# Kernel optimization log

Measured on AMD Instinct MI355X. Metric: run time of the kernel, lower is better.

Reference implementation:

```python
import jax, jax.numpy as jnp
import numpy as np

D_MODEL = 512
N_HEADS = 8
HEAD_DIM = D_MODEL // N_HEADS
D_FF = 2048
EPS = 1e-5


def layer_norm(x, gamma, beta):
    mu = jnp.mean(x, axis=-1, keepdims=True)
    var = jnp.mean((x - mu) ** 2, axis=-1, keepdims=True)
    return (x - mu) * jax.lax.rsqrt(var + EPS) * gamma + beta


def setup_inputs() -> dict:
    key = jax.random.key(0)
    ks = jax.random.split(key, 17)
    B, S = 2, 2048
    s_in = 1.0 / np.sqrt(D_MODEL)
    s_ff = 1.0 / np.sqrt(D_FF)
    return {
        "x": jax.random.normal(ks[0], (B, S, D_MODEL), jnp.float32),
        "Wq": jax.random.normal(ks[1], (D_MODEL, D_MODEL), jnp.float32) * s_in,
        "bq": jnp.zeros((D_MODEL,), jnp.float32),
        "Wk": jax.random.normal(ks[2], (D_MODEL, D_MODEL), jnp.float32) * s_in,
        "bk": jnp.zeros((D_MODEL,), jnp.float32),
        "Wv": jax.random.normal(ks[3], (D_MODEL, D_MODEL), jnp.float32) * s_in,
        "bv": jnp.zeros((D_MODEL,), jnp.float32),
        "Wo": jax.random.normal(ks[4], (D_MODEL, D_MODEL), jnp.float32) * s_in,
        "bo": jnp.zeros((D_MODEL,), jnp.float32),
        "W1": jax.random.normal(ks[5], (D_MODEL, D_FF), jnp.float32) * s_in,
        "b1": jnp.zeros((D_FF,), jnp.float32),
        "W2": jax.random.normal(ks[6], (D_FF, D_MODEL), jnp.float32) * s_ff,
        "b2": jnp.zeros((D_MODEL,), jnp.float32),
        "g1": jnp.ones((D_MODEL,), jnp.float32),
        "be1": jnp.zeros((D_MODEL,), jnp.float32),
        "g2": jnp.ones((D_MODEL,), jnp.float32),
        "be2": jnp.zeros((D_MODEL,), jnp.float32),
    }


def reference(x, Wq, bq, Wk, bk, Wv, bv, Wo, bo, W1, b1, W2, b2, g1, be1, g2, be2):
    B, S, _ = x.shape
    # projections + split heads -> [B, H, S, Dh]
    def heads(t):
        return t.reshape(B, S, N_HEADS, HEAD_DIM).transpose(0, 2, 1, 3)
    q = heads(x @ Wq + bq)
    k = heads(x @ Wk + bk)
    v = heads(x @ Wv + bv)
    # explicit scaled dot-product attention (full [B,H,S,S] scores as in source)
    scores = jnp.einsum('bhqd,bhkd->bhqk', q, k) / np.sqrt(HEAD_DIM).astype(np.float32)
    attn = jax.nn.softmax(scores, axis=-1)
    ctx = jnp.einsum('bhqk,bhkd->bhqd', attn, v)
    ctx = ctx.transpose(0, 2, 1, 3).reshape(B, S, D_MODEL)
    attn_out = ctx @ Wo + bo
    # post-norm residual 1
    h = layer_norm(x + attn_out, g1, be1)
    # FFN
    ff = jax.nn.relu(h @ W1 + b1) @ W2 + b2
    # post-norm residual 2
    return layer_norm(h + ff, g2, be2)
```

## Files before the change

### kernel.cpp

```cpp
#include <hip/hip_runtime.h>
#include <cmath>

#define D_MODEL 512
#define N_HEADS 8
#define HEAD_DIM 64
#define D_FF 2048
#define SEQ 2048
#define BATCH 2
#define MROWS (BATCH * SEQ)

typedef __attribute__((ext_vector_type(8))) short short8;
typedef __attribute__((ext_vector_type(4))) float float4v;
typedef unsigned short ushort_t;

static __device__ __forceinline__ ushort_t f2bf(float f) {
    union { float f; unsigned u; } v; v.f = f;
    unsigned r = (v.u + 0x7FFFu + ((v.u >> 16) & 1u)) >> 16;
    return (ushort_t)r;
}
static __device__ __forceinline__ ushort_t f2bf_trunc(float f) {
    union { float f; unsigned u; } v; v.f = f;
    return (ushort_t)(v.u >> 16);
}

static __device__ __forceinline__ void gload16(const void* g, void* l) {
    __builtin_amdgcn_global_load_lds(
        (__attribute__((address_space(1))) void*)(unsigned long long)g,
        (__attribute__((address_space(3))) void*)(unsigned)(unsigned long long)l,
        16, 0, 0);
}

__global__ __launch_bounds__(256) void xbf_k(const float* __restrict__ x,
                                             ushort_t* __restrict__ xb)
{
    int i = blockIdx.x * 256 + threadIdx.x;
    float4 f = ((const float4*)x)[i];
    ushort4 o;
    o.x = f2bf(f.x); o.y = f2bf(f.y); o.z = f2bf(f.z); o.w = f2bf(f.w);
    ((ushort4*)xb)[i] = o;
}

__global__ __launch_bounds__(256) void wt_k(
    const float* __restrict__ Wq, const float* __restrict__ Wk,
    const float* __restrict__ Wv, const float* __restrict__ Wo,
    const float* __restrict__ W1, const float* __restrict__ W2,
    ushort_t* __restrict__ WqkvT, ushort_t* __restrict__ WoT,
    ushort_t* __restrict__ W1T, ushort_t* __restrict__ W2T)
{
    int tile = blockIdx.x;
    const float* src; ushort_t* dst; int Kd, Nd, tloc;
    if (tile < 1024) {
        int wsel = tile >> 8; tloc = tile & 255; Kd = 512; Nd = 512;
        if (wsel == 0)      { src = Wq; dst = WqkvT; }
        else if (wsel == 1) { src = Wk; dst = WqkvT + (size_t)512 * 512; }
        else if (wsel == 2) { src = Wv; dst = WqkvT + (size_t)1024 * 512; }
        else                { src = Wo; dst = WoT; }
    } else if (tile < 2048) { tloc = tile - 1024; Kd = 512;  Nd = 2048; src = W1; dst = W1T; }
    else                    { tloc = tile - 2048; Kd = 2048; Nd = 512;  src = W2; dst = W2T; }
    int tn = Nd >> 5;
    int k0 = (tloc / tn) << 5, n0 = (tloc % tn) << 5;
    __shared__ float tl[32][33];
    int c = threadIdx.x & 31, r = threadIdx.x >> 5;
    #pragma unroll
    for (int i = 0; i < 4; ++i)
        tl[r + i * 8][c] = src[(size_t)(k0 + r + i * 8) * Nd + n0 + c];
    __syncthreads();
    #pragma unroll
    for (int i = 0; i < 4; ++i)
        dst[(size_t)(n0 + r + i * 8) * Kd + k0 + c] = f2bf(tl[c][r + i * 8]);
}

template <int BM, int BN, int WCOLS, int MT, int NT>
__device__ __forceinline__ void gemm_core(
    const ushort_t* __restrict__ A, const ushort_t* __restrict__ BT,
    int K, int kbase, int Klen, int m0, int n0, float4v (&acc)[MT][NT])
{
    __shared__ ushort_t As[BM * 32];
    __shared__ ushort_t Bs[BN * 32];

    const int t = threadIdx.x;
    const int w = t >> 6;
    const int lane = t & 63;
    const int l16 = lane & 15;
    const int quad = lane >> 4;
    const int mbase = (w / WCOLS) * (MT * 16);
    const int nbase = (w % WCOLS) * (NT * 16);
    const int lr = lane >> 2;
    const int lc = (lane & 3) * 8;

    for (int k0 = kbase; k0 < kbase + Klen; k0 += 32) {
        __syncthreads();
        for (int c = w; c < BM / 16; c += 4)
            gload16(A + (size_t)(m0 + c * 16 + lr) * K + k0 + lc, &As[c * 512]);
        for (int c = w; c < BN / 16; c += 4)
            gload16(BT + (size_t)(n0 + c * 16 + lr) * K + k0 + lc, &Bs[c * 512]);
        __syncthreads();

        short8 af[MT], bfr[NT];
        #pragma unroll
        for (int mt = 0; mt < MT; ++mt)
            af[mt] = *(const short8*)&As[(mbase + mt * 16 + l16) * 32 + quad * 8];
        #pragma unroll
        for (int nt = 0; nt < NT; ++nt)
            bfr[nt] = *(const short8*)&Bs[(nbase + nt * 16 + l16) * 32 + quad * 8];
        #pragma unroll
        for (int mt = 0; mt < MT; ++mt)
            #pragma unroll
            for (int nt = 0; nt < NT; ++nt)
                acc[mt][nt] = __builtin_amdgcn_mfma_f32_16x16x32_bf16(
                    af[mt], bfr[nt], acc[mt][nt], 0, 0, 0);
    }
}

template <int BM, int BN, int WCOLS, int MT, int NT, int MODE>
__global__ __launch_bounds__(256) void gemm_std_k(
    const ushort_t* __restrict__ A, const ushort_t* __restrict__ BT,
    const float* __restrict__ bias, void* __restrict__ Cv,
    int N, int K, int Klen, size_t zstride)
{
    const int m0 = blockIdx.y * BM;
    const int n0 = blockIdx.x * BN;
    const int kbase = blockIdx.z * Klen;
    float4v acc[MT][NT];
    #pragma unroll
    for (int mt = 0; mt < MT; ++mt)
        #pragma unroll
        for (int nt = 0; nt < NT; ++nt)
            acc[mt][nt] = (float4v){0.f, 0.f, 0.f, 0.f};
    gemm_core<BM, BN, WCOLS, MT, NT>(A, BT, K, kbase, Klen, m0, n0, acc);

    const int t = threadIdx.x;
    const int w = t >> 6, lane = t & 63, l16 = lane & 15, quad = lane >> 4;
    const int mbase = (w / WCOLS) * (MT * 16);
    const int nbase = (w % WCOLS) * (NT * 16);
    float* Cf = (float*)Cv + blockIdx.z * zstride;
    #pragma unroll
    for (int mt = 0; mt < MT; ++mt) {
        #pragma unroll
        for (int nt = 0; nt < NT; ++nt) {
            int gcol = n0 + nbase + nt * 16 + l16;
            float b = (MODE == 2) ? 0.f : bias[gcol];
            #pragma unroll
            for (int r = 0; r < 4; ++r) {
                int grow = m0 + mbase + mt * 16 + quad * 4 + r;
                float v = acc[mt][nt][r] + b;
                if (MODE == 1) v = fmaxf(v, 0.f);
                if (MODE == 1) ((ushort_t*)Cv)[(size_t)grow * N + gcol] = f2bf(v);
                else           Cf[(size_t)grow * N + gcol] = v;
            }
        }
    }
}

__global__ __launch_bounds__(256) void gemm_qkv_k(
    const ushort_t* __restrict__ A, const ushort_t* __restrict__ BT,
    const float* __restrict__ bq, const float* __restrict__ bk,
    const float* __restrict__ bv,
    ushort_t* __restrict__ Qb, ushort_t* __restrict__ Kb,
    ushort_t* __restrict__ VTb)
{
    const int m0 = blockIdx.y * 64;
    const int n0 = blockIdx.x * 128;
    float4v acc[2][4];
    #pragma unroll
    for (int mt = 0; mt < 2; ++mt)
        #pragma unroll
        for (int nt = 0; nt < 4; ++nt)
            acc[mt][nt] = (float4v){0.f, 0.f, 0.f, 0.f};
    gemm_core<64, 128, 2, 2, 4>(A, BT, 512, 0, 512, m0, n0, acc);

    const int t = threadIdx.x;
    const int w = t >> 6, lane = t & 63, l16 = lane & 15, quad = lane >> 4;
    const int mbase = (w >> 1) * 32;
    const int nbase = (w & 1) * 64;
    const int tsel = n0 >> 9;
    const float* bias = (tsel == 0) ? bq : (tsel == 1) ? bk : bv;
    const float scl = (tsel == 0) ? 0.18033688f : 1.0f;
    ushort_t* dst = (tsel == 0) ? Qb : Kb;

    #pragma unroll
    for (int mt = 0; mt < 2; ++mt) {
        #pragma unroll
        for (int nt = 0; nt < 4; ++nt) {
            int gcol = n0 + nbase + nt * 16 + l16;
            int lcol = gcol - (tsel << 9);
            int h = lcol >> 6, dh = lcol & 63;
            float b = bias[lcol];
            #pragma unroll
            for (int r = 0; r < 4; ++r) {
                int grow = m0 + mbase + mt * 16 + quad * 4 + r;
                int bb = grow >> 11, s = grow & 2047;
                float v = (acc[mt][nt][r] + b) * scl;
                if (tsel < 2)
                    dst[(((size_t)(bb * N_HEADS + h)) * SEQ + s) * HEAD_DIM + dh] = f2bf(v);
                else
                    VTb[(((size_t)(bb * N_HEADS + h)) * HEAD_DIM + dh) * SEQ + s] = f2bf(v);
            }
        }
    }
}

__global__ __launch_bounds__(256) void attn_mfma_k(
    const ushort_t* __restrict__ Qg, const ushort_t* __restrict__ Kg,
    const ushort_t* __restrict__ VTg,
    float* __restrict__ Opart, float* __restrict__ Lpart)
{
    __shared__ __align__(16) ushort_t Ks[64 * 72];
    __shared__ __align__(16) ushort_t Vs[64 * 72];
    __shared__ __align__(16) ushort_t Ps[4][16 * 76];

    const int bh = blockIdx.x;
    const int q0 = blockIdx.y * 64;
    const int ks = blockIdx.z;
    const int t = threadIdx.x;
    const int w = t >> 6;
    const int lane = t & 63;
    const int l16 = lane & 15;
    const int quad = lane >> 4;
    const int qbase = q0 + w * 16;
    const float M2 = 14.4269504f;

    short8 aq[2];
    {
        const ushort_t* qp = Qg + ((size_t)bh * SEQ + qbase + l16) * HEAD_DIM + quad * 8;
        aq[0] = *(const short8*)(qp);
        aq[1] = *(const short8*)(qp + 32);
    }

    float4v o[4] = {};
    float l_acc[4] = {0.f, 0.f, 0.f, 0.f};

    for (int kt = 0; kt < 16; ++kt) {
        const int kbase = ks * 1024 + kt * 64;
        __syncthreads();
        #pragma unroll
        for (int lit = 0; lit < 2; ++lit) {
            int flat = lit * 256 + t;
            int row = flat >> 3;
            int c0 = (flat & 7) * 8;
            *(short8*)&Ks[row * 72 + c0] =
                *(const short8*)(Kg + ((size_t)bh * SEQ + kbase + row) * HEAD_DIM + c0);
            *(short8*)&Vs[row * 72 + c0] =
                *(const short8*)(VTg + ((size_t)bh * HEAD_DIM + row) * SEQ + kbase + c0);
        }
        __syncthreads();

        float4v s[4];
        #pragma unroll
        for (int nt = 0; nt < 4; ++nt) s[nt] = (float4v){0.f, 0.f, 0.f, 0.f};
        #pragma unroll
        for (int c = 0; c < 2; ++c) {
            #pragma unroll
            for (int nt = 0; nt < 4; ++nt) {
                short8 bk8 = *(const short8*)&Ks[(nt * 16 + l16) * 72 + c * 32 + quad * 8];
                s[nt] = __builtin_amdgcn_mfma_f32_16x16x32_bf16(aq[c], bk8, s[nt], 0, 0, 0);
            }
        }

        #pragma unroll
        for (int nt = 0; nt < 4; ++nt) {
            #pragma unroll
            for (int r = 0; r < 4; ++r) {
                float p = exp2f(s[nt][r] - M2);
                s[nt][r] = p;
                l_acc[r] += p;
            }
        }

        #pragma unroll
        for (int nt = 0; nt < 4; ++nt)
            #pragma unroll
            for (int r = 0; r < 4; ++r)
                Ps[w][(quad * 4 + r) * 76 + nt * 16 + l16] = f2bf_trunc(s[nt][r]);
        asm volatile("s_waitcnt lgkmcnt(0)" ::: "memory");

        #pragma unroll
        for (int c = 0; c < 2; ++c) {
            short8 ap = *(const short8*)&Ps[w][l16 * 76 + c * 32 + quad * 8];
            #pragma unroll
            for (int dt = 0; dt < 4; ++dt) {
                short8 bv8 = *(const short8*)&Vs[(dt * 16 + l16) * 72 + c * 32 + quad * 8];
                o[dt] = __builtin_amdgcn_mfma_f32_16x16x32_bf16(ap, bv8, o[dt], 0, 0, 0);
            }
        }
    }

    const size_t pbase = ((size_t)(ks * 16 + bh)) * SEQ;
    #pragma unroll
    for (int r = 0; r < 4; ++r) {
        float L = l_acc[r];
        #pragma unroll
        for (int msk = 1; msk < 16; msk <<= 1) L += __shfl_xor(L, msk);
        int qrow = qbase + quad * 4 + r;
        if (l16 == 0) Lpart[pbase + qrow] = L;
        #pragma unroll
        for (int dt = 0; dt < 4; ++dt)
            Opart[(pbase + qrow) * HEAD_DIM + dt * 16 + l16] = o[dt][r];
    }
}

__global__ __launch_bounds__(256) void attn_comb_k(
    const float* __restrict__ Op, const float* __restrict__ Lp,
    ushort_t* __restrict__ ctx)
{
    int g = blockIdx.x * 256 + threadIdx.x;
    int d4 = g & 15;
    int q  = (g >> 4) & 2047;
    int bh = g >> 15;
    size_t rowa = ((size_t)bh * SEQ + q) * HEAD_DIM;
    size_t rowb = ((size_t)(16 + bh) * SEQ + q) * HEAD_DIM;
    float4 a = ((const float4*)(Op + rowa))[d4];
    float4 b = ((const float4*)(Op + rowb))[d4];
    float inv = 1.0f / (Lp[bh * SEQ + q] + Lp[16 * SEQ + bh * SEQ + q]);
    ushort4 o4;
    o4.x = f2bf((a.x + b.x) * inv);
    o4.y = f2bf((a.y + b.y) * inv);
    o4.z = f2bf((a.z + b.z) * inv);
    o4.w = f2bf((a.w + b.w) * inv);
    int bb = bh >> 3, hh = bh & 7;
    *(ushort4*)&ctx[((size_t)(bb * SEQ + q)) * D_MODEL + hh * HEAD_DIM + d4 * 4] = o4;
}

template <int WRITE_BF>
__global__ __launch_bounds__(256) void add_ln_k(
    const float* __restrict__ X, const float* __restrict__ P0,
    const float* __restrict__ P1, const float* __restrict__ bias,
    const float* __restrict__ gam, const float* __restrict__ bet,
    float* __restrict__ O, ushort_t* __restrict__ Ob)
{
    const int row = blockIdx.x;
    const int t = threadIdx.x;
    const size_t ro = (size_t)row * D_MODEL;

    float v0 = X[ro + t]       + P0[ro + t]       + P1[ro + t]       + bias[t];
    float v1 = X[ro + t + 256] + P0[ro + t + 256] + P1[ro + t + 256] + bias[t + 256];
    float s = v0 + v1;
    float ss = v0 * v0 + v1 * v1;
    #pragma unroll
    for (int off = 32; off > 0; off >>= 1) {
        s  += __shfl_down(s, off);
        ss += __shfl_down(ss, off);
    }
    __shared__ float sb[4], ssb[4];
    if ((t & 63) == 0) { sb[t >> 6] = s; ssb[t >> 6] = ss; }
    __syncthreads();
    float S  = sb[0] + sb[1] + sb[2] + sb[3];
    float SS = ssb[0] + ssb[1] + ssb[2] + ssb[3];
    float mu  = S * (1.0f / D_MODEL);
    float var = SS * (1.0f / D_MODEL) - mu * mu;
    float inv = rsqrtf(var + 1e-5f);
    float o0 = (v0 - mu) * inv * gam[t] + bet[t];
    float o1 = (v1 - mu) * inv * gam[t + 256] + bet[t + 256];
    O[ro + t]       = o0;
    O[ro + t + 256] = o1;
    if (WRITE_BF) {
        Ob[ro + t]       = f2bf(o0);
        Ob[ro + t + 256] = f2bf(o1);
    }
}

extern "C" void kernel_launch(void* const* d_in, const int* in_sizes, int n_in,
                              void* d_out, int out_size, void* d_ws, size_t ws_size,
                              hipStream_t stream)
{
    const float* x   = (const float*)d_in[0];
    const float* Wq  = (const float*)d_in[1];
    const float* bq  = (const float*)d_in[2];
    const float* Wk  = (const float*)d_in[3];
    const float* bk  = (const float*)d_in[4];
    const float* Wv  = (const float*)d_in[5];
    const float* bv  = (const float*)d_in[6];
    const float* Wo  = (const float*)d_in[7];
    const float* bo  = (const float*)d_in[8];
    const float* W1  = (const float*)d_in[9];
    const float* b1  = (const float*)d_in[10];
    const float* W2  = (const float*)d_in[11];
    const float* b2  = (const float*)d_in[12];
    const float* g1  = (const float*)d_in[13];
    const float* be1 = (const float*)d_in[14];
    const float* g2  = (const float*)d_in[15];
    const float* be2 = (const float*)d_in[16];
    float* out = (float*)d_out;
    float* ws  = (float*)d_ws;

    ushort_t* WoT   = (ushort_t*)(ws);
    ushort_t* W1T   = (ushort_t*)(ws + 131072);
    ushort_t* W2T   = (ushort_t*)(ws + 655360);
    ushort_t* WqkvT = (ushort_t*)(ws + 1179648);
    ushort_t* xb    = (ushort_t*)(ws + 1572864);
    ushort_t* Qb    = (ushort_t*)(ws + 2621440);
    ushort_t* Kb    = (ushort_t*)(ws + 3670016);
    ushort_t* VTb   = (ushort_t*)(ws + 4718592);
    ushort_t* Ctx   = (ushort_t*)(ws + 5767168);
    float*    Lpart = ws + 6815744;
    float*    Hh    = ws + 6881280;
    float*    P0    = ws + 8978432;
    float*    P1    = ws + 11075584;
    float*    Opart = ws + 8978432;
    ushort_t* FF1   = (ushort_t*)(ws + 1572864);
    ushort_t* Hhb   = (ushort_t*)(ws + 5767168);

    xbf_k<<<2048, 256, 0, stream>>>(x, xb);
    wt_k<<<3072, 256, 0, stream>>>(Wq, Wk, Wv, Wo, W1, W2, WqkvT, WoT, W1T, W2T);

    gemm_qkv_k<<<dim3(12, 64), 256, 0, stream>>>(xb, WqkvT, bq, bk, bv, Qb, Kb, VTb);

    attn_mfma_k<<<dim3(16, 32, 2), 256, 0, stream>>>(Qb, Kb, VTb, Opart, Lpart);
    attn_comb_k<<<2048, 256, 0, stream>>>(Opart, Lpart, Ctx);

    gemm_std_k<64, 64, 2, 2, 2, 2><<<dim3(8, 64, 2), 256, 0, stream>>>(
        Ctx, WoT, nullptr, P0, 512, 512, 256, (size_t)MROWS * D_MODEL);

    add_ln_k<1><<<4096, 256, 0, stream>>>(x, P0, P1, bo, g1, be1, Hh, Hhb);

    gemm_std_k<64, 128, 2, 2, 4, 1><<<dim3(16, 64), 256, 0, stream>>>(
        Hhb, W1T, b1, FF1, 2048, 512, 512, 0);

    gemm_std_k<64, 64, 2, 2, 2, 2><<<dim3(8, 64, 2), 256, 0, stream>>>(
        FF1, W2T, nullptr, P0, 512, 2048, 1024, (size_t)MROWS * D_MODEL);

    add_ln_k<0><<<4096, 256, 0, stream>>>(Hh, P0, P1, b2, g2, be2, out, (ushort_t*)nullptr);
}
```

Before: 232.7 us.

## Replace LDS GEMMs with direct-load register-pipelined GEMMs, split attention keys four ways

Several changes land together. The weight-transpose and x-to-bf16 kernels are merged into a single prep launch. Every GEMM drops the LDS-staged core in favour of wave-private direct global loads into registers, double-buffered across k steps (32x256 block tiles). The key split in attention goes from 2 to 4 partitions, with a matching 4-way combine, and the P scratch in LDS uses an XOR swizzle in place of padding. The workspace offsets are moved so the larger Opart buffer fits. The aim is to cut launch count, barrier overhead and LDS bank conflicts and to raise attention parallelism. The cost is that A and B operands are no longer shared through LDS, so the GEMMs issue more redundant global and L2 reads, and the combine pass moves more partial data.

```diff
diff --git a/kernel.cpp b/kernel.cpp
--- a/kernel.cpp
+++ b/kernel.cpp
@@ -23,31 +23,24 @@
     return (ushort_t)(v.u >> 16);
 }
 
-static __device__ __forceinline__ void gload16(const void* g, void* l) {
-    __builtin_amdgcn_global_load_lds(
-        (__attribute__((address_space(1))) void*)(unsigned long long)g,
-        (__attribute__((address_space(3))) void*)(unsigned)(unsigned long long)l,
-        16, 0, 0);
-}
-
-__global__ __launch_bounds__(256) void xbf_k(const float* __restrict__ x,
-                                             ushort_t* __restrict__ xb)
-{
-    int i = blockIdx.x * 256 + threadIdx.x;
-    float4 f = ((const float4*)x)[i];
-    ushort4 o;
-    o.x = f2bf(f.x); o.y = f2bf(f.y); o.z = f2bf(f.z); o.w = f2bf(f.w);
-    ((ushort4*)xb)[i] = o;
-}
-
-__global__ __launch_bounds__(256) void wt_k(
+__global__ __launch_bounds__(256) void prep_k(
+    const float* __restrict__ x,
     const float* __restrict__ Wq, const float* __restrict__ Wk,
     const float* __restrict__ Wv, const float* __restrict__ Wo,
     const float* __restrict__ W1, const float* __restrict__ W2,
+    ushort_t* __restrict__ xb,
     ushort_t* __restrict__ WqkvT, ushort_t* __restrict__ WoT,
     ushort_t* __restrict__ W1T, ushort_t* __restrict__ W2T)
 {
     int tile = blockIdx.x;
+    if (tile >= 3072) {
+        int i = (tile - 3072) * 256 + threadIdx.x;
+        float4 f = ((const float4*)x)[i];
+        ushort4 o;
+        o.x = f2bf(f.x); o.y = f2bf(f.y); o.z = f2bf(f.z); o.w = f2bf(f.w);
+        ((ushort4*)xb)[i] = o;
+        return;
+    }
     const float* src; ushort_t* dst; int Kd, Nd, tloc;
     if (tile < 1024) {
         int wsel = tile >> 8; tloc = tile & 255; Kd = 512; Nd = 512;
@@ -70,79 +63,68 @@
         dst[(size_t)(n0 + r + i * 8) * Kd + k0 + c] = f2bf(tl[c][r + i * 8]);
 }
 
-template <int BM, int BN, int WCOLS, int MT, int NT>
-__device__ __forceinline__ void gemm_core(
-    const ushort_t* __restrict__ A, const ushort_t* __restrict__ BT,
-    int K, int kbase, int Klen, int m0, int n0, float4v (&acc)[MT][NT])
-{
-    __shared__ ushort_t As[BM * 32];
-    __shared__ ushort_t Bs[BN * 32];
-
-    const int t = threadIdx.x;
-    const int w = t >> 6;
-    const int lane = t & 63;
-    const int l16 = lane & 15;
-    const int quad = lane >> 4;
-    const int mbase = (w / WCOLS) * (MT * 16);
-    const int nbase = (w % WCOLS) * (NT * 16);
-    const int lr = lane >> 2;
-    const int lc = (lane & 3) * 8;
-
-    for (int k0 = kbase; k0 < kbase + Klen; k0 += 32) {
-        __syncthreads();
-        for (int c = w; c < BM / 16; c += 4)
-            gload16(A + (size_t)(m0 + c * 16 + lr) * K + k0 + lc, &As[c * 512]);
-        for (int c = w; c < BN / 16; c += 4)
-            gload16(BT + (size_t)(n0 + c * 16 + lr) * K + k0 + lc, &Bs[c * 512]);
-        __syncthreads();
-
-        short8 af[MT], bfr[NT];
-        #pragma unroll
-        for (int mt = 0; mt < MT; ++mt)
-            af[mt] = *(const short8*)&As[(mbase + mt * 16 + l16) * 32 + quad * 8];
-        #pragma unroll
-        for (int nt = 0; nt < NT; ++nt)
-            bfr[nt] = *(const short8*)&Bs[(nbase + nt * 16 + l16) * 32 + quad * 8];
-        #pragma unroll
-        for (int mt = 0; mt < MT; ++mt)
-            #pragma unroll
-            for (int nt = 0; nt < NT; ++nt)
-                acc[mt][nt] = __builtin_amdgcn_mfma_f32_16x16x32_bf16(
-                    af[mt], bfr[nt], acc[mt][nt], 0, 0, 0);
-    }
-}
-
-template <int BM, int BN, int WCOLS, int MT, int NT, int MODE>
-__global__ __launch_bounds__(256) void gemm_std_k(
+#define DL_LOAD(buf, koff)                                                     \
+    {                                                                          \
+        _Pragma("unroll")                                                      \
+        for (int mt = 0; mt < 2; ++mt)                                         \
+            af[buf][mt] = *(const short8*)(Ap + (size_t)mt * 16 * K + (koff)); \
+        _Pragma("unroll")                                                      \
+        for (int nt = 0; nt < 4; ++nt)                                         \
+            bf8[buf][nt] = *(const short8*)(Bp + (size_t)nt * 16 * K + (koff));\
+    }
+#define DL_MFMA(buf)                                                           \
+    {                                                                          \
+        _Pragma("unroll")                                                      \
+        for (int mt = 0; mt < 2; ++mt)                                         \
+            _Pragma("unroll")                                                  \
+            for (int nt = 0; nt < 4; ++nt)                                     \
+                acc[mt][nt] = __builtin_amdgcn_mfma_f32_16x16x32_bf16(         \
+                    af[buf][mt], bf8[buf][nt], acc[mt][nt], 0, 0, 0);          \
+    }
+
+template <int MODE>
+__global__ __launch_bounds__(256) void gemm_dl_k(
     const ushort_t* __restrict__ A, const ushort_t* __restrict__ BT,
     const float* __restrict__ bias, void* __restrict__ Cv,
     int N, int K, int Klen, size_t zstride)
 {
-    const int m0 = blockIdx.y * BM;
-    const int n0 = blockIdx.x * BN;
-    const int kbase = blockIdx.z * Klen;
-    float4v acc[MT][NT];
-    #pragma unroll
-    for (int mt = 0; mt < MT; ++mt)
-        #pragma unroll
-        for (int nt = 0; nt < NT; ++nt)
-            acc[mt][nt] = (float4v){0.f, 0.f, 0.f, 0.f};
-    gemm_core<BM, BN, WCOLS, MT, NT>(A, BT, K, kbase, Klen, m0, n0, acc);
-
     const int t = threadIdx.x;
     const int w = t >> 6, lane = t & 63, l16 = lane & 15, quad = lane >> 4;
-    const int mbase = (w / WCOLS) * (MT * 16);
-    const int nbase = (w % WCOLS) * (NT * 16);
+    const int m0 = blockIdx.y * 32;
+    const int n0 = blockIdx.x * 256 + w * 64;
+    const int kbase = blockIdx.z * Klen;
+
+    const ushort_t* Ap = A + (size_t)(m0 + l16) * K + kbase + quad * 8;
+    const ushort_t* Bp = BT + (size_t)(n0 + l16) * K + kbase + quad * 8;
+
+    float4v acc[2][4];
+    #pragma unroll
+    for (int mt = 0; mt < 2; ++mt)
+        #pragma unroll
+        for (int nt = 0; nt < 4; ++nt)
+            acc[mt][nt] = (float4v){0.f, 0.f, 0.f, 0.f};
+
+    short8 af[2][2], bf8[2][4];
+    DL_LOAD(0, 0)
+    const int nsteps = Klen >> 6;
+    for (int kk = 0; kk < nsteps; ++kk) {
+        const int k = kk << 6;
+        DL_LOAD(1, k + 32)
+        DL_MFMA(0)
+        if (kk + 1 < nsteps) DL_LOAD(0, k + 64)
+        DL_MFMA(1)
+    }
+
     float* Cf = (float*)Cv + blockIdx.z * zstride;
     #pragma unroll
-    for (int mt = 0; mt < MT; ++mt) {
-        #pragma unroll
-        for (int nt = 0; nt < NT; ++nt) {
-            int gcol = n0 + nbase + nt * 16 + l16;
+    for (int mt = 0; mt < 2; ++mt) {
+        #pragma unroll
+        for (int nt = 0; nt < 4; ++nt) {
+            int gcol = n0 + nt * 16 + l16;
             float b = (MODE == 2) ? 0.f : bias[gcol];
             #pragma unroll
             for (int r = 0; r < 4; ++r) {
-                int grow = m0 + mbase + mt * 16 + quad * 4 + r;
+                int grow = m0 + mt * 16 + quad * 4 + r;
                 float v = acc[mt][nt][r] + b;
                 if (MODE == 1) v = fmaxf(v, 0.f);
                 if (MODE == 1) ((ushort_t*)Cv)[(size_t)grow * N + gcol] = f2bf(v);
@@ -152,27 +134,39 @@
     }
 }
 
-__global__ __launch_bounds__(256) void gemm_qkv_k(
+__global__ __launch_bounds__(256) void gemm_dl_qkv(
     const ushort_t* __restrict__ A, const ushort_t* __restrict__ BT,
     const float* __restrict__ bq, const float* __restrict__ bk,
     const float* __restrict__ bv,
     ushort_t* __restrict__ Qb, ushort_t* __restrict__ Kb,
     ushort_t* __restrict__ VTb)
 {
-    const int m0 = blockIdx.y * 64;
-    const int n0 = blockIdx.x * 128;
+    const int t = threadIdx.x;
+    const int w = t >> 6, lane = t & 63, l16 = lane & 15, quad = lane >> 4;
+    const int m0 = blockIdx.y * 32;
+    const int n0 = blockIdx.x * 256 + w * 64;
+    const int K = 512;
+
+    const ushort_t* Ap = A + (size_t)(m0 + l16) * K + quad * 8;
+    const ushort_t* Bp = BT + (size_t)(n0 + l16) * K + quad * 8;
+
     float4v acc[2][4];
     #pragma unroll
     for (int mt = 0; mt < 2; ++mt)
         #pragma unroll
         for (int nt = 0; nt < 4; ++nt)
             acc[mt][nt] = (float4v){0.f, 0.f, 0.f, 0.f};
-    gemm_core<64, 128, 2, 2, 4>(A, BT, 512, 0, 512, m0, n0, acc);
-
-    const int t = threadIdx.x;
-    const int w = t >> 6, lane = t & 63, l16 = lane & 15, quad = lane >> 4;
-    const int mbase = (w >> 1) * 32;
-    const int nbase = (w & 1) * 64;
+
+    short8 af[2][2], bf8[2][4];
+    DL_LOAD(0, 0)
+    for (int kk = 0; kk < 8; ++kk) {
+        const int k = kk << 6;
+        DL_LOAD(1, k + 32)
+        DL_MFMA(0)
+        if (kk + 1 < 8) DL_LOAD(0, k + 64)
+        DL_MFMA(1)
+    }
+
     const int tsel = n0 >> 9;
     const float* bias = (tsel == 0) ? bq : (tsel == 1) ? bk : bv;
     const float scl = (tsel == 0) ? 0.18033688f : 1.0f;
@@ -182,13 +176,13 @@
     for (int mt = 0; mt < 2; ++mt) {
         #pragma unroll
         for (int nt = 0; nt < 4; ++nt) {
-            int gcol = n0 + nbase + nt * 16 + l16;
+            int gcol = n0 + nt * 16 + l16;
             int lcol = gcol - (tsel << 9);
             int h = lcol >> 6, dh = lcol & 63;
             float b = bias[lcol];
             #pragma unroll
             for (int r = 0; r < 4; ++r) {
-                int grow = m0 + mbase + mt * 16 + quad * 4 + r;
+                int grow = m0 + mt * 16 + quad * 4 + r;
                 int bb = grow >> 11, s = grow & 2047;
                 float v = (acc[mt][nt][r] + b) * scl;
                 if (tsel < 2)
@@ -207,7 +201,7 @@
 {
     __shared__ __align__(16) ushort_t Ks[64 * 72];
     __shared__ __align__(16) ushort_t Vs[64 * 72];
-    __shared__ __align__(16) ushort_t Ps[4][16 * 76];
+    __shared__ __align__(16) ushort_t Ps[4][16 * 64];
 
     const int bh = blockIdx.x;
     const int q0 = blockIdx.y * 64;
@@ -230,8 +224,8 @@
     float4v o[4] = {};
     float l_acc[4] = {0.f, 0.f, 0.f, 0.f};
 
-    for (int kt = 0; kt < 16; ++kt) {
-        const int kbase = ks * 1024 + kt * 64;
+    for (int kt = 0; kt < 8; ++kt) {
+        const int kbase = ks * 512 + kt * 64;
         __syncthreads();
         #pragma unroll
         for (int lit = 0; lit < 2; ++lit) {
@@ -270,13 +264,17 @@
         #pragma unroll
         for (int nt = 0; nt < 4; ++nt)
             #pragma unroll
-            for (int r = 0; r < 4; ++r)
-                Ps[w][(quad * 4 + r) * 76 + nt * 16 + l16] = f2bf_trunc(s[nt][r]);
+            for (int r = 0; r < 4; ++r) {
+                int row = quad * 4 + r;
+                int key = nt * 16 + l16;
+                Ps[w][row * 64 + (((key >> 3) ^ (row & 7)) << 3) + (key & 7)] =
+                    f2bf_trunc(s[nt][r]);
+            }
         asm volatile("s_waitcnt lgkmcnt(0)" ::: "memory");
 
         #pragma unroll
         for (int c = 0; c < 2; ++c) {
-            short8 ap = *(const short8*)&Ps[w][l16 * 76 + c * 32 + quad * 8];
+            short8 ap = *(const short8*)&Ps[w][l16 * 64 + ((((c << 2) + quad) ^ (l16 & 7)) << 3)];
             #pragma unroll
             for (int dt = 0; dt < 4; ++dt) {
                 short8 bv8 = *(const short8*)&Vs[(dt * 16 + l16) * 72 + c * 32 + quad * 8];
@@ -307,16 +305,20 @@
     int d4 = g & 15;
     int q  = (g >> 4) & 2047;
     int bh = g >> 15;
-    size_t rowa = ((size_t)bh * SEQ + q) * HEAD_DIM;
-    size_t rowb = ((size_t)(16 + bh) * SEQ + q) * HEAD_DIM;
-    float4 a = ((const float4*)(Op + rowa))[d4];
-    float4 b = ((const float4*)(Op + rowb))[d4];
-    float inv = 1.0f / (Lp[bh * SEQ + q] + Lp[16 * SEQ + bh * SEQ + q]);
+    float ax = 0.f, ay = 0.f, az = 0.f, aw = 0.f, L = 0.f;
+    #pragma unroll
+    for (int ks = 0; ks < 4; ++ks) {
+        size_t row = ((size_t)(ks * 16 + bh) * SEQ + q) * HEAD_DIM;
+        float4 a = ((const float4*)(Op + row))[d4];
+        ax += a.x; ay += a.y; az += a.z; aw += a.w;
+        L += Lp[ks * 16 * SEQ + bh * SEQ + q];
+    }
+    float inv = 1.0f / L;
     ushort4 o4;
-    o4.x = f2bf((a.x + b.x) * inv);
-    o4.y = f2bf((a.y + b.y) * inv);
-    o4.z = f2bf((a.z + b.z) * inv);
-    o4.w = f2bf((a.w + b.w) * inv);
+    o4.x = f2bf(ax * inv);
+    o4.y = f2bf(ay * inv);
+    o4.z = f2bf(az * inv);
+    o4.w = f2bf(aw * inv);
     int bb = bh >> 3, hh = bh & 7;
     *(ushort4*)&ctx[((size_t)(bb * SEQ + q)) * D_MODEL + hh * HEAD_DIM + d4 * 4] = o4;
 }
@@ -393,30 +395,29 @@
     ushort_t* VTb   = (ushort_t*)(ws + 4718592);
     ushort_t* Ctx   = (ushort_t*)(ws + 5767168);
     float*    Lpart = ws + 6815744;
-    float*    Hh    = ws + 6881280;
-    float*    P0    = ws + 8978432;
-    float*    P1    = ws + 11075584;
-    float*    Opart = ws + 8978432;
+    float*    Opart = ws + 6946816;
+    float*    Hh    = ws + 6946816;
+    float*    P0    = ws + 9043968;
+    float*    P1    = ws + 11141120;
     ushort_t* FF1   = (ushort_t*)(ws + 1572864);
     ushort_t* Hhb   = (ushort_t*)(ws + 5767168);
 
-    xbf_k<<<2048, 256, 0, stream>>>(x, xb);
-    wt_k<<<3072, 256, 0, stream>>>(Wq, Wk, Wv, Wo, W1, W2, WqkvT, WoT, W1T, W2T);
-
-    gemm_qkv_k<<<dim3(12, 64), 256, 0, stream>>>(xb, WqkvT, bq, bk, bv, Qb, Kb, VTb);
-
-    attn_mfma_k<<<dim3(16, 32, 2), 256, 0, stream>>>(Qb, Kb, VTb, Opart, Lpart);
+    prep_k<<<5120, 256, 0, stream>>>(x, Wq, Wk, Wv, Wo, W1, W2, xb, WqkvT, WoT, W1T, W2T);
+
+    gemm_dl_qkv<<<dim3(6, 128), 256, 0, stream>>>(xb, WqkvT, bq, bk, bv, Qb, Kb, VTb);
+
+    attn_mfma_k<<<dim3(16, 32, 4), 256, 0, stream>>>(Qb, Kb, VTb, Opart, Lpart);
     attn_comb_k<<<2048, 256, 0, stream>>>(Opart, Lpart, Ctx);
 
-    gemm_std_k<64, 64, 2, 2, 2, 2><<<dim3(8, 64, 2), 256, 0, stream>>>(
+    gemm_dl_k<2><<<dim3(2, 128, 2), 256, 0, stream>>>(
         Ctx, WoT, nullptr, P0, 512, 512, 256, (size_t)MROWS * D_MODEL);
 
     add_ln_k<1><<<4096, 256, 0, stream>>>(x, P0, P1, bo, g1, be1, Hh, Hhb);
 
-    gemm_std_k<64, 128, 2, 2, 4, 1><<<dim3(16, 64), 256, 0, stream>>>(
+    gemm_dl_k<1><<<dim3(8, 128), 256, 0, stream>>>(
         Hhb, W1T, b1, FF1, 2048, 512, 512, 0);
 
-    gemm_std_k<64, 64, 2, 2, 2, 2><<<dim3(8, 64, 2), 256, 0, stream>>>(
+    gemm_dl_k<2><<<dim3(2, 128, 2), 256, 0, stream>>>(
         FF1, W2T, nullptr, P0, 512, 2048, 1024, (size_t)MROWS * D_MODEL);
 
     add_ln_k<0><<<4096, 256, 0, stream>>>(Hh, P0, P1, b2, g2, be2, out, (ushort_t*)nullptr);
```

After: 313.5 us. 1.35x slower.
